# Kernel tuning notes

Measured on AMD Instinct MI355X. Metric: run time of the kernel, lower is better.

The kernel has to match this reference:

```python
import jax, jax.numpy as jnp
import numpy as np
import math

E = 1024   # embedding_size
H = 16     # layer_size (num heads)
DK = 64    # key_size
DH = 64    # head_size
HID = 4096 # hidden_size
B = 2
S = 2048   # context_size
EPS = 1e-5


def layer_norm(x, w, b):
    mu = jnp.mean(x, axis=-1, keepdims=True)
    var = jnp.mean(jnp.square(x - mu), axis=-1, keepdims=True)
    return (x - mu) * jax.lax.rsqrt(var + EPS) * w + b


def setup_inputs() -> dict:
    key = jax.random.key(0)
    ks = jax.random.split(key, 16)
    sE = 1.0 / math.sqrt(E)
    sH = 1.0 / math.sqrt(HID)
    return {
        "embeddings": jax.random.normal(ks[0], (B, S, E), dtype=jnp.float32),
        "Wq": jax.random.uniform(ks[1], (H, E, DK), minval=-sE, maxval=sE, dtype=jnp.float32),
        "bq": jnp.zeros((H, DK), dtype=jnp.float32),
        "Wk": jax.random.uniform(ks[2], (H, E, DK), minval=-sE, maxval=sE, dtype=jnp.float32),
        "bk": jnp.zeros((H, DK), dtype=jnp.float32),
        "Wv": jax.random.uniform(ks[3], (H, E, DH), minval=-sE, maxval=sE, dtype=jnp.float32),
        "bv": jnp.zeros((H, DH), dtype=jnp.float32),
        "ln1_w": jnp.ones((E,), dtype=jnp.float32),
        "ln1_b": jnp.zeros((E,), dtype=jnp.float32),
        "ln2_w": jnp.ones((E,), dtype=jnp.float32),
        "ln2_b": jnp.zeros((E,), dtype=jnp.float32),
        "W1": jax.random.uniform(ks[4], (E, HID), minval=-sE, maxval=sE, dtype=jnp.float32),
        "b1": jnp.zeros((HID,), dtype=jnp.float32),
        "W2": jax.random.uniform(ks[5], (HID, E), minval=-sH, maxval=sH, dtype=jnp.float32),
        "b2": jnp.zeros((E,), dtype=jnp.float32),
    }


def reference(embeddings, Wq, bq, Wk, bk, Wv, bv, ln1_w, ln1_b, ln2_w, ln2_b, W1, b1, W2, b2):
    # NOTE: faithful to source: residual uses the POST-norm activations
    # (embeddings is reassigned to the LayerNorm output before the residual add).
    x = layer_norm(embeddings, ln1_w, ln1_b)            # [B,S,E]
    q = jnp.einsum('bse,hed->bhsd', x, Wq) + bq[:, None, :]
    k = jnp.einsum('bse,hed->bhsd', x, Wk) + bk[:, None, :]
    v = jnp.einsum('bse,hed->bhsd', x, Wv) + bv[:, None, :]
    scores = jnp.einsum('bhsd,bhtd->bhst', q, k) / math.sqrt(DK)  # [B,H,S,S]
    causal = jnp.tril(jnp.ones((S, S), dtype=bool))
    scores = jnp.where(causal, scores, -jnp.inf)
    w = jax.nn.softmax(scores, axis=-1)
    o = jnp.einsum('bhst,bhtd->bhsd', w, v)             # [B,H,S,DH]
    o = jnp.transpose(o, (0, 2, 1, 3)).reshape(B, S, H * DH)  # concat heads
    x = x + o
    y = layer_norm(x, ln2_w, ln2_b)
    h = jax.nn.relu(jnp.einsum('bse,eh->bsh', y, W1) + b1)
    out = y + jnp.einsum('bsh,he->bse', h, W2) + b2
    return out
```

## Files before the change

### kernel.cpp

```cpp
#include <hip/hip_runtime.h>


typedef unsigned short u16;
typedef unsigned int   u32;
typedef __bf16 bf16x8 __attribute__((ext_vector_type(8)));
typedef float  f32x4  __attribute__((ext_vector_type(4)));

#define NEG_INF (-__builtin_inff())

#if __has_builtin(__builtin_amdgcn_exp2f)
#define EXP2F(x) __builtin_amdgcn_exp2f(x)
#else
#define EXP2F(x) exp2f(x)
#endif

__device__ __forceinline__ u32 pack_bf16_trunc(float a, float b) {
#if __has_builtin(__builtin_amdgcn_perm)
  return __builtin_amdgcn_perm(__float_as_uint(b), __float_as_uint(a), 0x07060302u);
#else
  return (__float_as_uint(a) >> 16) | (__float_as_uint(b) & 0xFFFF0000u);
#endif
}

__device__ __forceinline__ u16 f2b(float f) {
  u32 u = __float_as_uint(f);
  u = (u + 0x7fffu + ((u >> 16) & 1u)) >> 16;
  return (u16)u;
}

__device__ __forceinline__ void gload16(const void* g, void* l) {
  __builtin_amdgcn_global_load_lds(
      (const __attribute__((address_space(1))) u32*)g,
      (__attribute__((address_space(3))) u32*)l, 16, 0, 0);
}

__device__ __forceinline__ bf16x8 ld16(const u16* p) { return *(const bf16x8*)p; }

__global__ __launch_bounds__(256)
void transpose_qkv_k(const float* __restrict__ Wq, const float* __restrict__ Wk,
                     const float* __restrict__ Wv, u16* __restrict__ out) {
  __shared__ float tile[64][65];
  int z = blockIdx.z, which = z >> 4, sub = z & 15;
  const float* in = which == 0 ? Wq : (which == 1 ? Wk : Wv);
  const float* ip = in + (size_t)sub * 1024 * 64;
  u16* op = out + (size_t)which * 1024 * 1024 + (size_t)sub * 64 * 1024;
  int r0 = blockIdx.x * 64;
  int tr = threadIdx.x >> 6, tc = threadIdx.x & 63;
#pragma unroll
  for (int i = 0; i < 16; i++) {
    int r = i * 4 + tr;
    tile[r][tc] = ip[(size_t)(r0 + r) * 64 + tc];
  }
  __syncthreads();
#pragma unroll
  for (int i = 0; i < 16; i++) {
    int c = i * 4 + tr;
    op[(size_t)c * 1024 + r0 + tc] = f2b(tile[tc][c]);
  }
}

__global__ __launch_bounds__(256)
void transpose_w12_k(const float* __restrict__ W1, const float* __restrict__ W2,
                     u16* __restrict__ W1t, u16* __restrict__ W2t) {
  __shared__ float tile[64][65];
  int id = blockIdx.x;
  const float* in; u16* out; int R, C, r0, c0;
  if (id < 1024) { in = W1; out = W1t; R = 1024; C = 4096; r0 = (id & 15) * 64; c0 = (id >> 4) * 64; }
  else { id -= 1024; in = W2; out = W2t; R = 4096; C = 1024; r0 = (id >> 4) * 64; c0 = (id & 15) * 64; }
  int tr = threadIdx.x >> 6, tc = threadIdx.x & 63;
#pragma unroll
  for (int i = 0; i < 16; i++) {
    int r = i * 4 + tr;
    tile[r][tc] = in[(size_t)(r0 + r) * C + c0 + tc];
  }
  __syncthreads();
#pragma unroll
  for (int i = 0; i < 16; i++) {
    int c = i * 4 + tr;
    out[(size_t)(c0 + c) * R + r0 + tc] = f2b(tile[tc][c]);
  }
}

__global__ __launch_bounds__(256)
void vtrans_k(const u16* __restrict__ vin, u16* __restrict__ vt) {
  __shared__ __align__(16) u16 tile[64][72];
  int s0 = blockIdx.x * 64, bh = blockIdx.y;
  const u16* ip = vin + (size_t)bh * 2048 * 64;
  u16* op = vt + (size_t)bh * 64 * 2048;
  int t = threadIdx.x;
#pragma unroll
  for (int i = 0; i < 2; i++) {
    int idx = i * 256 + t, r = idx >> 3, c = idx & 7;
    *(uint4*)&tile[r][c * 8] = *(const uint4*)(ip + (size_t)(s0 + r) * 64 + c * 8);
  }
  __syncthreads();
#pragma unroll
  for (int i = 0; i < 16; i++) {
    int d = i * 4 + (t >> 6), s = t & 63;
    op[(size_t)d * 2048 + s0 + s] = tile[s][d];
  }
}

__global__ __launch_bounds__(256)
void ln_k(const float* __restrict__ in, const float* __restrict__ in2,
          const float* __restrict__ w, const float* __restrict__ b,
          float* __restrict__ outf, u16* __restrict__ outb) {
  int row = blockIdx.x, t = threadIdx.x;
  const float4* ip = (const float4*)(in + (size_t)row * 1024);
  float4 x = ip[t];
  if (in2) {
    const float4* ip2 = (const float4*)(in2 + (size_t)row * 1024);
    float4 o = ip2[t];
    x.x += o.x; x.y += o.y; x.z += o.z; x.w += o.w;
  }
  float s = x.x + x.y + x.z + x.w;
  float q = x.x * x.x + x.y * x.y + x.z * x.z + x.w * x.w;
#pragma unroll
  for (int m = 32; m; m >>= 1) { s += __shfl_xor(s, m); q += __shfl_xor(q, m); }
  __shared__ float rs[4], rq[4];
  if ((t & 63) == 0) { rs[t >> 6] = s; rq[t >> 6] = q; }
  __syncthreads();
  s = rs[0] + rs[1] + rs[2] + rs[3];
  q = rq[0] + rq[1] + rq[2] + rq[3];
  float mean = s * (1.f / 1024.f);
  float var  = q * (1.f / 1024.f) - mean * mean;
  float rstd = rsqrtf(var + 1e-5f);
  float4 wv = ((const float4*)w)[t];
  float4 bv = ((const float4*)b)[t];
  float4 y;
  y.x = (x.x - mean) * rstd * wv.x + bv.x;
  y.y = (x.y - mean) * rstd * wv.y + bv.y;
  y.z = (x.z - mean) * rstd * wv.z + bv.z;
  y.w = (x.w - mean) * rstd * wv.w + bv.w;
  if (outf) ((float4*)(outf + (size_t)row * 1024))[t] = y;
  ushort4 ub;
  ub.x = f2b(y.x); ub.y = f2b(y.y); ub.z = f2b(y.z); ub.w = f2b(y.w);
  ((ushort4*)(outb + (size_t)row * 1024))[t] = ub;
}

#define EPI_QKV  0
#define EPI_RELU 1
#define EPI_RES  2

#define QSCALE 0.18033688011112042f

template <int EPI>
__device__ __forceinline__
void gemm_body(const u16* __restrict__ A, const u16* __restrict__ Bt,
               int K, int lda, int ldbt,
               const float* __restrict__ bias0, const float* __restrict__ bias1,
               const float* __restrict__ bias2, const float* __restrict__ res,
               int ldout, u16* __restrict__ outb, float* __restrict__ outf,
               float* __restrict__ outp) {
  __shared__ __align__(16) u16 As[128 * 64];
  __shared__ __align__(16) u16 Bs[128 * 64];
  int t = threadIdx.x;
  int wave = t >> 6, lane = t & 63, quad = lane >> 4, l16 = lane & 15;
  int x7 = l16 & 7;
  int wm = (wave >> 1) * 64, wn = (wave & 1) * 64;
  int bm = blockIdx.x * 128, bn = blockIdx.y * 128;
  int zoff = blockIdx.z * K;

  const u16* Agl[4];
  const u16* Bgl[4];
#pragma unroll
  for (int i = 0; i < 4; i++) {
    int idx = i * 256 + t, r = idx >> 3, c = (idx & 7) ^ (r & 7);
    Agl[i] = A + (size_t)(bm + r) * lda + zoff + c * 8;
    Bgl[i] = Bt + (size_t)(bn + r) * ldbt + zoff + c * 8;
  }
  u16* Asl = As + t * 8;
  u16* Bsl = Bs + t * 8;

  f32x4 acc[4][4] = {};

  for (int k0 = 0; k0 < K; k0 += 64) {
#pragma unroll
    for (int i = 0; i < 4; i++) {
      gload16(Agl[i] + k0, Asl + i * 2048);
      gload16(Bgl[i] + k0, Bsl + i * 2048);
    }
    __syncthreads();
#pragma unroll
    for (int kc = 0; kc < 2; kc++) {
      bf16x8 af[4], bfr[4];
#pragma unroll
      for (int i = 0; i < 4; i++) {
        int r = wm + i * 16 + l16;
        af[i] = *(const bf16x8*)(As + r * 64 + (((kc * 4 + quad) ^ x7) * 8));
      }
#pragma unroll
      for (int j = 0; j < 4; j++) {
        int r = wn + j * 16 + l16;
        bfr[j] = *(const bf16x8*)(Bs + r * 64 + (((kc * 4 + quad) ^ x7) * 8));
      }
#pragma unroll
      for (int i = 0; i < 4; i++)
#pragma unroll
        for (int j = 0; j < 4; j++)
          acc[i][j] = __builtin_amdgcn_mfma_f32_16x16x32_bf16(af[i], bfr[j],
                                                              acc[i][j], 0, 0, 0);
    }
    __syncthreads();
  }

#pragma unroll
  for (int i = 0; i < 4; i++) {
#pragma unroll
    for (int j = 0; j < 4; j++) {
      int c = bn + wn + j * 16 + l16;
#pragma unroll
      for (int rr = 0; rr < 4; rr++) {
        int r = bm + wm + i * 16 + quad * 4 + rr;
        float v = acc[i][j][rr];
        if (EPI == EPI_QKV) {
          int which = c >> 10, h = (c >> 6) & 15, d = c & 63;
          const float* bp = which == 0 ? bias0 : (which == 1 ? bias1 : bias2);
          v += bp[h * 64 + d];
          if (which == 0) v *= QSCALE;
          int bb = r >> 11, ss = r & 2047;
          outb[((size_t)(which * 32 + bb * 16 + h) * 2048 + ss) * 64 + d] = f2b(v);
        } else if (EPI == EPI_RELU) {
          v += bias0[c];
          v = v > 0.f ? v : 0.f;
          outb[(size_t)r * ldout + c] = f2b(v);
        } else {
          if (blockIdx.z == 0) {
            v += bias0[c] + res[(size_t)r * ldout + c];
            outf[(size_t)r * ldout + c] = v;
          } else {
            outp[(size_t)r * ldout + c] = v;
          }
        }
      }
    }
  }
}

__global__ __launch_bounds__(256)
void qkv_gemm(const u16* A, const u16* Bt, int K, int lda, int ldbt,
              const float* b0, const float* b1, const float* b2,
              u16* outb) {
  gemm_body<EPI_QKV>(A, Bt, K, lda, ldbt, b0, b1, b2, nullptr, 0, outb, nullptr, nullptr);
}
__global__ __launch_bounds__(256)
void ffn1_gemm(const u16* A, const u16* Bt, int K, int lda, int ldbt,
               const float* b0, int ldout, u16* outb) {
  gemm_body<EPI_RELU>(A, Bt, K, lda, ldbt, b0, nullptr, nullptr, nullptr, ldout, outb, nullptr, nullptr);
}
__global__ __launch_bounds__(256)
void ffn2_gemm(const u16* A, const u16* Bt, int K, int lda, int ldbt,
               const float* b0, const float* res, int ldout,
               float* outf, float* outp) {
  gemm_body<EPI_RES>(A, Bt, K, lda, ldbt, b0, nullptr, nullptr, res, ldout, nullptr, outf, outp);
}

__global__ __launch_bounds__(256)
void reduce_k(float* __restrict__ out, const float* __restrict__ part) {
  int i = blockIdx.x * 256 + threadIdx.x;
  float4 a = ((const float4*)part)[i];
  float4 b = ((float4*)out)[i];
  b.x += a.x; b.y += a.y; b.z += a.z; b.w += a.w;
  ((float4*)out)[i] = b;
}

__global__ __launch_bounds__(512, 6)
void attn_k(const u16* __restrict__ qkv, const u16* __restrict__ vt,
            float* __restrict__ o) {
  int bh = blockIdx.y, b = bh >> 4, h = bh & 15;
  int Qt = b ? (15 - (int)blockIdx.x) : (int)blockIdx.x;
  int t = threadIdx.x;
  int wave = t >> 6, lane = t & 63, quad = lane >> 4, l16 = lane & 15;
  int x7 = l16 & 7;
  int q0 = Qt * 128 + wave * 16;

  const u16* qg = qkv + (size_t)bh * (2048 * 64);
  const u16* kg = qkv + (size_t)(32 + bh) * (2048 * 64);
  const u16* vg = vt + (size_t)bh * (64 * 2048);

  __shared__ __align__(16) u16 Ks[2][64 * 64];
  __shared__ __align__(16) u16 Vs[2][64 * 64];
  __shared__ __align__(16) u16 Ps[8][16 * 64 + 32];
  u16* Pw = Ps[wave];
  float* auxf = (float*)(Pw + 1024);

  int sr = t >> 3, sc_ = (t & 7) ^ (sr & 7);

  gload16(kg + (size_t)sr * 64 + sc_ * 8, Ks[0] + t * 8);
  gload16(vg + (size_t)sr * 2048 + sc_ * 8, Vs[0] + t * 8);

  bf16x8 qf0 = ld16(qg + (size_t)(q0 + l16) * 64 + quad * 8);
  bf16x8 qf1 = ld16(qg + (size_t)(q0 + l16) * 64 + 32 + quad * 8);

  f32x4 oacc[4] = {};
  float mo = NEG_INF, ll = 0.f;
  int kmax_w = q0 >> 6;
  int klast = 2 * Qt + 1;

  __syncthreads();

  for (int kt = 0; kt <= klast; kt++) {
    const u16* ks = Ks[kt & 1];
    const u16* vs = Vs[kt & 1];
    if (kt < klast) {
      gload16(kg + (size_t)((kt + 1) * 64 + sr) * 64 + sc_ * 8, Ks[(kt + 1) & 1] + t * 8);
      gload16(vg + (size_t)sr * 2048 + (kt + 1) * 64 + sc_ * 8, Vs[(kt + 1) & 1] + t * 8);
    }
    if (kt <= kmax_w) {
      f32x4 sc[4];
#pragma unroll
      for (int g = 0; g < 4; g++) {
        const u16* kr = ks + (g * 16 + l16) * 64;
        bf16x8 kf0 = *(const bf16x8*)(kr + ((quad ^ x7) * 8));
        bf16x8 kf1 = *(const bf16x8*)(kr + (((4 + quad) ^ x7) * 8));
        f32x4 s = {};
        s = __builtin_amdgcn_mfma_f32_16x16x32_bf16(kf0, qf0, s, 0, 0, 0);
        s = __builtin_amdgcn_mfma_f32_16x16x32_bf16(kf1, qf1, s, 0, 0, 0);
        sc[g] = s;
      }

      if (kt == kmax_w) {
#pragma unroll
        for (int g = 0; g < 4; g++) {
          int kvb = kt * 64 + g * 16 + quad * 4;
#pragma unroll
          for (int rr = 0; rr < 4; rr++)
            if (kvb + rr > q0 + l16) sc[g][rr] = NEG_INF;
        }
      }

      float mx = sc[0][0];
#pragma unroll
      for (int g = 0; g < 4; g++)
#pragma unroll
        for (int rr = 0; rr < 4; rr++) mx = fmaxf(mx, sc[g][rr]);
      mx = fmaxf(mx, __shfl_xor(mx, 16));
      mx = fmaxf(mx, __shfl_xor(mx, 32));
      float mnew = fmaxf(mo, mx);
      float al = EXP2F(mo - mnew);
      mo = mnew;

      float sum = 0.f;
#pragma unroll
      for (int g = 0; g < 4; g++) {
        float p0 = EXP2F(sc[g][0] - mnew);
        float p1 = EXP2F(sc[g][1] - mnew);
        float p2 = EXP2F(sc[g][2] - mnew);
        float p3 = EXP2F(sc[g][3] - mnew);
        sum += (p0 + p1) + (p2 + p3);
        u32 lo = pack_bf16_trunc(p0, p1);
        u32 hi = pack_bf16_trunc(p2, p3);
        int slot = (2 * g + (quad >> 1)) ^ x7;
        *(uint2*)(Pw + l16 * 64 + slot * 8 + (quad & 1) * 4) = make_uint2(lo, hi);
      }
      sum += __shfl_xor(sum, 16);
      sum += __shfl_xor(sum, 32);
      ll = ll * al + sum;

      if (lane < 16) auxf[lane] = al;
      f32x4 av = *(const f32x4*)(auxf + quad * 4);
#pragma unroll
      for (int g = 0; g < 4; g++)
#pragma unroll
        for (int rr = 0; rr < 4; rr++) oacc[g][rr] *= av[rr];

      bf16x8 pf0 = *(const bf16x8*)(Pw + l16 * 64 + ((quad ^ x7) * 8));
      bf16x8 pf1 = *(const bf16x8*)(Pw + l16 * 64 + (((4 + quad) ^ x7) * 8));
#pragma unroll
      for (int g = 0; g < 4; g++) {
        const u16* vr = vs + (g * 16 + l16) * 64;
        bf16x8 vf0 = *(const bf16x8*)(vr + ((quad ^ x7) * 8));
        bf16x8 vf1 = *(const bf16x8*)(vr + (((4 + quad) ^ x7) * 8));
        oacc[g] = __builtin_amdgcn_mfma_f32_16x16x32_bf16(pf0, vf0, oacc[g], 0, 0, 0);
        oacc[g] = __builtin_amdgcn_mfma_f32_16x16x32_bf16(pf1, vf1, oacc[g], 0, 0, 0);
      }
    }
    __syncthreads();
  }

  if (lane < 16) auxf[lane] = ll;
  f32x4 lv = *(const f32x4*)(auxf + quad * 4);
  float rinv[4];
#pragma unroll
  for (int rr = 0; rr < 4; rr++) rinv[rr] = 1.f / lv[rr];
  float* op = o + ((size_t)b * 2048 + q0) * 1024 + h * 64;
#pragma unroll
  for (int g = 0; g < 4; g++)
#pragma unroll
    for (int rr = 0; rr < 4; rr++)
      op[(size_t)(quad * 4 + rr) * 1024 + g * 16 + l16] = oacc[g][rr] * rinv[rr];
}

extern "C" void kernel_launch(void* const* d_in, const int* in_sizes, int n_in,
                              void* d_out, int out_size, void* d_ws, size_t ws_size,
                              hipStream_t stream) {
  const float* emb  = (const float*)d_in[0];
  const float* Wq   = (const float*)d_in[1];
  const float* bq   = (const float*)d_in[2];
  const float* Wk   = (const float*)d_in[3];
  const float* bk   = (const float*)d_in[4];
  const float* Wv   = (const float*)d_in[5];
  const float* bv   = (const float*)d_in[6];
  const float* ln1w = (const float*)d_in[7];
  const float* ln1b = (const float*)d_in[8];
  const float* ln2w = (const float*)d_in[9];
  const float* ln2b = (const float*)d_in[10];
  const float* W1   = (const float*)d_in[11];
  const float* b1   = (const float*)d_in[12];
  const float* W2   = (const float*)d_in[13];
  const float* b2   = (const float*)d_in[14];
  float* out = (float*)d_out;

  char* p = (char*)d_ws;
  u16*   Wqkv_t = (u16*)p;   p += (size_t)3072 * 1024 * 2;
  u16*   W1t    = (u16*)p;   p += (size_t)4096 * 1024 * 2;
  u16*   W2t    = (u16*)p;   p += (size_t)1024 * 4096 * 2;
  float* x      = (float*)p; p += (size_t)4096 * 1024 * 4;
  u16*   xb     = (u16*)p;   p += (size_t)4096 * 1024 * 2;
  u16*   qkvb   = (u16*)p;   p += (size_t)3 * 32 * 2048 * 64 * 2;
  float* ob     = (float*)p; p += (size_t)4096 * 1024 * 4;
  float* y      = (float*)p; p += (size_t)4096 * 1024 * 4;
  u16*   yb     = (u16*)p;   p += (size_t)4096 * 1024 * 2;
  u16*   hb     = (u16*)qkvb;
  u16*   vT     = (u16*)y;
  float* part   = x;
  if (ws_size < (size_t)(p - (char*)d_ws)) return;

  transpose_qkv_k<<<dim3(16, 1, 48), 256, 0, stream>>>(Wq, Wk, Wv, Wqkv_t);
  transpose_w12_k<<<dim3(2048), 256, 0, stream>>>(W1, W2, W1t, W2t);

  ln_k<<<dim3(4096), 256, 0, stream>>>(emb, nullptr, ln1w, ln1b, x, xb);

  qkv_gemm<<<dim3(32, 24, 1), 256, 0, stream>>>(
      xb, Wqkv_t, 1024, 1024, 1024, bq, bk, bv, qkvb);

  vtrans_k<<<dim3(32, 32), 256, 0, stream>>>(qkvb + (size_t)64 * 2048 * 64, vT);

  attn_k<<<dim3(16, 32), 512, 0, stream>>>(qkvb, vT, ob);

  ln_k<<<dim3(4096), 256, 0, stream>>>(x, ob, ln2w, ln2b, y, yb);

  ffn1_gemm<<<dim3(32, 32, 1), 256, 0, stream>>>(
      yb, W1t, 1024, 1024, 1024, b1, 4096, hb);

  ffn2_gemm<<<dim3(32, 8, 2), 256, 0, stream>>>(
      hb, W2t, 2048, 4096, 4096, b2, y, 1024, out, part);

  reduce_k<<<dim3(4096), 256, 0, stream>>>(out, part);
}
```

Measured before the change: 333.1 us.

## Merge prologue kernels, overlap W1/W2 transposes with QKV GEMM, split FFN2 K three ways

LayerNorm1 and the Wqkv transpose now run in one launch, and the W1/W2 transposes are folded into the QKV GEMM launch as extra blocks, so the grid fills with independent work and there are fewer kernel launches. The FFN2 split-K grows from 2 to 3 slices (1408/1344/1344) to give more blocks on 256 CUs. Partial sums go to reused workspace regions (the W1t area after FFN1, and the upper half of x). This costs an extra partial buffer read in the reduction and changes the workspace layout.

```diff
diff --git a/kernel.cpp b/kernel.cpp
--- a/kernel.cpp
+++ b/kernel.cpp
@@ -36,76 +36,11 @@
 
 __device__ __forceinline__ bf16x8 ld16(const u16* p) { return *(const bf16x8*)p; }
 
-__global__ __launch_bounds__(256)
-void transpose_qkv_k(const float* __restrict__ Wq, const float* __restrict__ Wk,
-                     const float* __restrict__ Wv, u16* __restrict__ out) {
-  __shared__ float tile[64][65];
-  int z = blockIdx.z, which = z >> 4, sub = z & 15;
-  const float* in = which == 0 ? Wq : (which == 1 ? Wk : Wv);
-  const float* ip = in + (size_t)sub * 1024 * 64;
-  u16* op = out + (size_t)which * 1024 * 1024 + (size_t)sub * 64 * 1024;
-  int r0 = blockIdx.x * 64;
-  int tr = threadIdx.x >> 6, tc = threadIdx.x & 63;
-#pragma unroll
-  for (int i = 0; i < 16; i++) {
-    int r = i * 4 + tr;
-    tile[r][tc] = ip[(size_t)(r0 + r) * 64 + tc];
-  }
-  __syncthreads();
-#pragma unroll
-  for (int i = 0; i < 16; i++) {
-    int c = i * 4 + tr;
-    op[(size_t)c * 1024 + r0 + tc] = f2b(tile[tc][c]);
-  }
-}
-
-__global__ __launch_bounds__(256)
-void transpose_w12_k(const float* __restrict__ W1, const float* __restrict__ W2,
-                     u16* __restrict__ W1t, u16* __restrict__ W2t) {
-  __shared__ float tile[64][65];
-  int id = blockIdx.x;
-  const float* in; u16* out; int R, C, r0, c0;
-  if (id < 1024) { in = W1; out = W1t; R = 1024; C = 4096; r0 = (id & 15) * 64; c0 = (id >> 4) * 64; }
-  else { id -= 1024; in = W2; out = W2t; R = 4096; C = 1024; r0 = (id >> 4) * 64; c0 = (id & 15) * 64; }
-  int tr = threadIdx.x >> 6, tc = threadIdx.x & 63;
-#pragma unroll
-  for (int i = 0; i < 16; i++) {
-    int r = i * 4 + tr;
-    tile[r][tc] = in[(size_t)(r0 + r) * C + c0 + tc];
-  }
-  __syncthreads();
-#pragma unroll
-  for (int i = 0; i < 16; i++) {
-    int c = i * 4 + tr;
-    out[(size_t)(c0 + c) * R + r0 + tc] = f2b(tile[tc][c]);
-  }
-}
-
-__global__ __launch_bounds__(256)
-void vtrans_k(const u16* __restrict__ vin, u16* __restrict__ vt) {
-  __shared__ __align__(16) u16 tile[64][72];
-  int s0 = blockIdx.x * 64, bh = blockIdx.y;
-  const u16* ip = vin + (size_t)bh * 2048 * 64;
-  u16* op = vt + (size_t)bh * 64 * 2048;
+__device__ __forceinline__
+void ln_body(int row, const float* __restrict__ in, const float* __restrict__ in2,
+             const float* __restrict__ w, const float* __restrict__ b,
+             float* __restrict__ outf, u16* __restrict__ outb) {
   int t = threadIdx.x;
-#pragma unroll
-  for (int i = 0; i < 2; i++) {
-    int idx = i * 256 + t, r = idx >> 3, c = idx & 7;
-    *(uint4*)&tile[r][c * 8] = *(const uint4*)(ip + (size_t)(s0 + r) * 64 + c * 8);
-  }
-  __syncthreads();
-#pragma unroll
-  for (int i = 0; i < 16; i++) {
-    int d = i * 4 + (t >> 6), s = t & 63;
-    op[(size_t)d * 2048 + s0 + s] = tile[s][d];
-  }
-}
-
-__global__ __launch_bounds__(256)
-void ln_k(const float* __restrict__ in, const float* __restrict__ in2,
-          const float* __restrict__ w, const float* __restrict__ b,
-          float* __restrict__ outf, u16* __restrict__ outb) {
-  int row = blockIdx.x, t = threadIdx.x;
   const float4* ip = (const float4*)(in + (size_t)row * 1024);
   float4 x = ip[t];
   if (in2) {
@@ -138,6 +73,70 @@
   ((ushort4*)(outb + (size_t)row * 1024))[t] = ub;
 }
 
+__device__ __forceinline__
+void trans_body(float* tile, const float* __restrict__ in, u16* __restrict__ out,
+                int R, int C, int r0, int c0) {
+  int tr = threadIdx.x >> 6, tc = threadIdx.x & 63;
+#pragma unroll
+  for (int i = 0; i < 16; i++) {
+    int r = i * 4 + tr;
+    tile[r * 65 + tc] = in[(size_t)(r0 + r) * C + c0 + tc];
+  }
+  __syncthreads();
+#pragma unroll
+  for (int i = 0; i < 16; i++) {
+    int c = i * 4 + tr;
+    out[(size_t)(c0 + c) * R + r0 + tc] = f2b(tile[tc * 65 + c]);
+  }
+}
+
+__global__ __launch_bounds__(256)
+void prologue_k(const float* __restrict__ emb, const float* __restrict__ ln1w,
+                const float* __restrict__ ln1b, float* __restrict__ x,
+                u16* __restrict__ xb, const float* __restrict__ Wq,
+                const float* __restrict__ Wk, const float* __restrict__ Wv,
+                u16* __restrict__ Wqkv_t) {
+  __shared__ float tile[64 * 65];
+  int bx = blockIdx.x;
+  if (bx < 4096) {
+    ln_body(bx, emb, nullptr, ln1w, ln1b, x, xb);
+  } else {
+    int id = bx - 4096;
+    int z = id >> 4, sub = z & 15, which = z >> 4;
+    const float* in = which == 0 ? Wq : (which == 1 ? Wk : Wv);
+    trans_body(tile, in + (size_t)sub * 1024 * 64,
+               Wqkv_t + (size_t)which * 1024 * 1024 + (size_t)sub * 64 * 1024,
+               1024, 64, (id & 15) * 64, 0);
+  }
+}
+
+__global__ __launch_bounds__(256)
+void vtrans_k(const u16* __restrict__ vin, u16* __restrict__ vt) {
+  __shared__ __align__(16) u16 tile[64][72];
+  int s0 = blockIdx.x * 64, bh = blockIdx.y;
+  const u16* ip = vin + (size_t)bh * 2048 * 64;
+  u16* op = vt + (size_t)bh * 64 * 2048;
+  int t = threadIdx.x;
+#pragma unroll
+  for (int i = 0; i < 2; i++) {
+    int idx = i * 256 + t, r = idx >> 3, c = idx & 7;
+    *(uint4*)&tile[r][c * 8] = *(const uint4*)(ip + (size_t)(s0 + r) * 64 + c * 8);
+  }
+  __syncthreads();
+#pragma unroll
+  for (int i = 0; i < 16; i++) {
+    int d = i * 4 + (t >> 6), s = t & 63;
+    op[(size_t)d * 2048 + s0 + s] = tile[s][d];
+  }
+}
+
+__global__ __launch_bounds__(256)
+void ln_k(const float* __restrict__ in, const float* __restrict__ in2,
+          const float* __restrict__ w, const float* __restrict__ b,
+          float* __restrict__ outf, u16* __restrict__ outb) {
+  ln_body(blockIdx.x, in, in2, w, b, outf, outb);
+}
+
 #define EPI_QKV  0
 #define EPI_RELU 1
 #define EPI_RES  2
@@ -146,35 +145,33 @@
 
 template <int EPI>
 __device__ __forceinline__
-void gemm_body(const u16* __restrict__ A, const u16* __restrict__ Bt,
-               int K, int lda, int ldbt,
+void gemm_body(u16* __restrict__ As, u16* __restrict__ Bs,
+               const u16* __restrict__ A, const u16* __restrict__ Bt,
+               int bxm, int bxn, int kbeg, int klen, int lda, int ldbt,
                const float* __restrict__ bias0, const float* __restrict__ bias1,
                const float* __restrict__ bias2, const float* __restrict__ res,
                int ldout, u16* __restrict__ outb, float* __restrict__ outf,
-               float* __restrict__ outp) {
-  __shared__ __align__(16) u16 As[128 * 64];
-  __shared__ __align__(16) u16 Bs[128 * 64];
+               float* __restrict__ p1, float* __restrict__ p2, int z) {
   int t = threadIdx.x;
   int wave = t >> 6, lane = t & 63, quad = lane >> 4, l16 = lane & 15;
   int x7 = l16 & 7;
   int wm = (wave >> 1) * 64, wn = (wave & 1) * 64;
-  int bm = blockIdx.x * 128, bn = blockIdx.y * 128;
-  int zoff = blockIdx.z * K;
+  int bm = bxm * 128, bn = bxn * 128;
 
   const u16* Agl[4];
   const u16* Bgl[4];
 #pragma unroll
   for (int i = 0; i < 4; i++) {
     int idx = i * 256 + t, r = idx >> 3, c = (idx & 7) ^ (r & 7);
-    Agl[i] = A + (size_t)(bm + r) * lda + zoff + c * 8;
-    Bgl[i] = Bt + (size_t)(bn + r) * ldbt + zoff + c * 8;
+    Agl[i] = A + (size_t)(bm + r) * lda + kbeg + c * 8;
+    Bgl[i] = Bt + (size_t)(bn + r) * ldbt + kbeg + c * 8;
   }
   u16* Asl = As + t * 8;
   u16* Bsl = Bs + t * 8;
 
   f32x4 acc[4][4] = {};
 
-  for (int k0 = 0; k0 < K; k0 += 64) {
+  for (int k0 = 0; k0 < klen; k0 += 64) {
 #pragma unroll
     for (int i = 0; i < 4; i++) {
       gload16(Agl[i] + k0, Asl + i * 2048);
@@ -225,11 +222,13 @@
           v = v > 0.f ? v : 0.f;
           outb[(size_t)r * ldout + c] = f2b(v);
         } else {
-          if (blockIdx.z == 0) {
+          if (z == 0) {
             v += bias0[c] + res[(size_t)r * ldout + c];
             outf[(size_t)r * ldout + c] = v;
+          } else if (z == 1) {
+            p1[(size_t)r * ldout + c] = v;
           } else {
-            outp[(size_t)r * ldout + c] = v;
+            p2[(size_t)r * ldout + c] = v;
           }
         }
       }
@@ -238,29 +237,60 @@
 }
 
 __global__ __launch_bounds__(256)
-void qkv_gemm(const u16* A, const u16* Bt, int K, int lda, int ldbt,
-              const float* b0, const float* b1, const float* b2,
-              u16* outb) {
-  gemm_body<EPI_QKV>(A, Bt, K, lda, ldbt, b0, b1, b2, nullptr, 0, outb, nullptr, nullptr);
-}
-__global__ __launch_bounds__(256)
-void ffn1_gemm(const u16* A, const u16* Bt, int K, int lda, int ldbt,
-               const float* b0, int ldout, u16* outb) {
-  gemm_body<EPI_RELU>(A, Bt, K, lda, ldbt, b0, nullptr, nullptr, nullptr, ldout, outb, nullptr, nullptr);
-}
-__global__ __launch_bounds__(256)
-void ffn2_gemm(const u16* A, const u16* Bt, int K, int lda, int ldbt,
-               const float* b0, const float* res, int ldout,
-               float* outf, float* outp) {
-  gemm_body<EPI_RES>(A, Bt, K, lda, ldbt, b0, nullptr, nullptr, res, ldout, nullptr, outf, outp);
-}
-
-__global__ __launch_bounds__(256)
-void reduce_k(float* __restrict__ out, const float* __restrict__ part) {
+void qkv_plus_k(const u16* __restrict__ xb, const u16* __restrict__ Wqkv_t,
+                const float* __restrict__ bq, const float* __restrict__ bk,
+                const float* __restrict__ bv, u16* __restrict__ qkvb,
+                const float* __restrict__ W1, const float* __restrict__ W2,
+                u16* __restrict__ W1t, u16* __restrict__ W2t) {
+  __shared__ __align__(16) u16 SM[2][128 * 64];
+  int bx = blockIdx.x;
+  if (bx < 768) {
+    gemm_body<EPI_QKV>(SM[0], SM[1], xb, Wqkv_t, bx & 31, bx >> 5, 0, 1024,
+                       1024, 1024, bq, bk, bv, nullptr, 0, qkvb, nullptr,
+                       nullptr, nullptr, 0);
+  } else {
+    int id = bx - 768;
+    float* tile = (float*)SM;
+    if (id < 1024)
+      trans_body(tile, W1, W1t, 1024, 4096, (id & 15) * 64, (id >> 4) * 64);
+    else {
+      id -= 1024;
+      trans_body(tile, W2, W2t, 4096, 1024, (id >> 4) * 64, (id & 15) * 64);
+    }
+  }
+}
+
+__global__ __launch_bounds__(256)
+void ffn1_gemm(const u16* __restrict__ A, const u16* __restrict__ Bt,
+               const float* __restrict__ b0, u16* __restrict__ outb) {
+  __shared__ __align__(16) u16 SM[2][128 * 64];
+  gemm_body<EPI_RELU>(SM[0], SM[1], A, Bt, blockIdx.x, blockIdx.y, 0, 1024,
+                      1024, 1024, b0, nullptr, nullptr, nullptr, 4096, outb,
+                      nullptr, nullptr, nullptr, 0);
+}
+
+__global__ __launch_bounds__(256)
+void ffn2_gemm(const u16* __restrict__ A, const u16* __restrict__ Bt,
+               const float* __restrict__ b0, const float* __restrict__ res,
+               float* __restrict__ outf, float* __restrict__ p1,
+               float* __restrict__ p2) {
+  __shared__ __align__(16) u16 SM[2][128 * 64];
+  int z = blockIdx.z;
+  int kbeg = z * 1344 + (z > 0 ? 64 : 0);
+  int klen = 1344 + (z == 0 ? 64 : 0);
+  gemm_body<EPI_RES>(SM[0], SM[1], A, Bt, blockIdx.x, blockIdx.y, kbeg, klen,
+                     4096, 4096, b0, nullptr, nullptr, res, 1024, nullptr,
+                     outf, p1, p2, z);
+}
+
+__global__ __launch_bounds__(256)
+void reduce2_k(float* __restrict__ out, const float* __restrict__ p1,
+               const float* __restrict__ p2) {
   int i = blockIdx.x * 256 + threadIdx.x;
-  float4 a = ((const float4*)part)[i];
+  float4 a = ((const float4*)p1)[i];
+  float4 c = ((const float4*)p2)[i];
   float4 b = ((float4*)out)[i];
-  b.x += a.x; b.y += a.y; b.z += a.z; b.w += a.w;
+  b.x += a.x + c.x; b.y += a.y + c.y; b.z += a.z + c.z; b.w += a.w + c.w;
   ((float4*)out)[i] = b;
 }
 
@@ -413,8 +443,8 @@
 
   char* p = (char*)d_ws;
   u16*   Wqkv_t = (u16*)p;   p += (size_t)3072 * 1024 * 2;
+  u16*   W2t    = (u16*)p;   p += (size_t)1024 * 4096 * 2;
   u16*   W1t    = (u16*)p;   p += (size_t)4096 * 1024 * 2;
-  u16*   W2t    = (u16*)p;   p += (size_t)1024 * 4096 * 2;
   float* x      = (float*)p; p += (size_t)4096 * 1024 * 4;
   u16*   xb     = (u16*)p;   p += (size_t)4096 * 1024 * 2;
   u16*   qkvb   = (u16*)p;   p += (size_t)3 * 32 * 2048 * 64 * 2;
@@ -423,16 +453,15 @@
   u16*   yb     = (u16*)p;   p += (size_t)4096 * 1024 * 2;
   u16*   hb     = (u16*)qkvb;
   u16*   vT     = (u16*)y;
-  float* part   = x;
+  float* part1  = (float*)W1t;
+  float* part2  = (float*)((char*)x + (size_t)4096 * 1024 * 2);
   if (ws_size < (size_t)(p - (char*)d_ws)) return;
 
-  transpose_qkv_k<<<dim3(16, 1, 48), 256, 0, stream>>>(Wq, Wk, Wv, Wqkv_t);
-  transpose_w12_k<<<dim3(2048), 256, 0, stream>>>(W1, W2, W1t, W2t);
-
-  ln_k<<<dim3(4096), 256, 0, stream>>>(emb, nullptr, ln1w, ln1b, x, xb);
-
-  qkv_gemm<<<dim3(32, 24, 1), 256, 0, stream>>>(
-      xb, Wqkv_t, 1024, 1024, 1024, bq, bk, bv, qkvb);
+  prologue_k<<<dim3(4096 + 768), 256, 0, stream>>>(
+      emb, ln1w, ln1b, x, xb, Wq, Wk, Wv, Wqkv_t);
+
+  qkv_plus_k<<<dim3(768 + 2048), 256, 0, stream>>>(
+      xb, Wqkv_t, bq, bk, bv, qkvb, W1, W2, W1t, W2t);
 
   vtrans_k<<<dim3(32, 32), 256, 0, stream>>>(qkvb + (size_t)64 * 2048 * 64, vT);
 
@@ -440,11 +469,9 @@
 
   ln_k<<<dim3(4096), 256, 0, stream>>>(x, ob, ln2w, ln2b, y, yb);
 
-  ffn1_gemm<<<dim3(32, 32, 1), 256, 0, stream>>>(
-      yb, W1t, 1024, 1024, 1024, b1, 4096, hb);
-
-  ffn2_gemm<<<dim3(32, 8, 2), 256, 0, stream>>>(
-      hb, W2t, 2048, 4096, 4096, b2, y, 1024, out, part);
-
-  reduce_k<<<dim3(4096), 256, 0, stream>>>(out, part);
-}
+  ffn1_gemm<<<dim3(32, 32), 256, 0, stream>>>(yb, W1t, b1, hb);
+
+  ffn2_gemm<<<dim3(32, 8, 3), 256, 0, stream>>>(hb, W2t, b2, y, out, part1, part2);
+
+  reduce2_k<<<dim3(4096), 256, 0, stream>>>(out, part1, part2);
+}
```

Measured after the change: 336.0 us. No clear change (+0.9%).
